# Kernel optimization log

Hardware: AMD Instinct MI355X
Metric: run time of the kernel (lower is better)

Reference implementation:

```python
import jax, jax.numpy as jnp
import numpy as np

B, S, D = 8, 1024, 1024
H, HD = 16, 64  # multiheads, head_dim; H*HD == D


def setup_inputs() -> dict:
    key = jax.random.key(0)
    ks = jax.random.split(key, 6)
    mk = lambda k, shape, scale=1.0: (jax.random.normal(k, shape, dtype=jnp.float32) * scale)
    return {
        "Q_seq": mk(ks[0], (B, S, D)),
        "K_seq": mk(ks[1], (B, S, D)),
        "V_seq": mk(ks[2], (B, S, D)),
        # nn.Linear weights stored as (out_features, in_features)
        "WQ": mk(ks[3], (H * HD, D), scale=D ** -0.5),
        "WK": mk(ks[4], (H * HD, D), scale=D ** -0.5),
        "WV": mk(ks[5], (H * HD, D), scale=D ** -0.5),
    }


def _attn(Q_seq, K_seq, V_seq, WQ, WK, WV):
    # projections (Linear: x @ W.T), then split heads -> [B, H, S, HD]
    def proj(x, W):
        y = jnp.einsum('bsd,od->bso', x, W)
        return y.reshape(x.shape[0], -1, H, HD).transpose(0, 2, 1, 3)
    Q, K, V = proj(Q_seq, WQ), proj(K_seq, WK), proj(V_seq, WV)
    scale = 1.0 / jnp.sqrt(jnp.float32(HD))
    scores = jnp.einsum('bhqd,bhkd->bhqk', Q, K) * scale  # [B,H,S,S]
    attn = jax.nn.softmax(scores, axis=-1)
    # dropout p=0.1 is identity in eval mode
    out = jnp.einsum('bhqk,bhkd->bhqd', attn, V)
    return out.transpose(0, 2, 1, 3).reshape(out.shape[0], -1, H * HD)


def reference(Q_seq, K_seq, V_seq, WQ, WK, WV):
    return _attn(Q_seq, K_seq, V_seq, WQ, WK, WV)
```

## Files before the change

### kernel.cpp

```cpp
#include <hip/hip_runtime.h>
#include <stdint.h>


#define B_N 8
#define S_N 1024
#define D_N 1024
#define H_N 16
#define HD_N 64
#define M_N (B_N * S_N)

typedef __bf16 bfrag __attribute__((ext_vector_type(8)));
typedef float f32x2 __attribute__((ext_vector_type(2)));
typedef float f32x4 __attribute__((ext_vector_type(4)));
typedef float f32x16 __attribute__((ext_vector_type(16)));
typedef unsigned int u32;
typedef u32 u32x2 __attribute__((ext_vector_type(2)));
typedef u32 u32x4 __attribute__((ext_vector_type(4)));
typedef unsigned short u16;

__device__ __forceinline__ u16 f2bf(float f) {
  uint32_t u = __float_as_uint(f);
  u += 0x7FFFu + ((u >> 16) & 1u);
  return (u16)(u >> 16);
}

__device__ __forceinline__ void gl_lds16(const void* g, void* l) {
  __builtin_amdgcn_global_load_lds(
      (const __attribute__((address_space(1))) uint32_t*)g,
      (__attribute__((address_space(3))) uint32_t*)l, 16, 0, 0);
}

__device__ __forceinline__ u32 cvtpk(float lo, float hi) {
  u32 r;
  asm("v_cvt_pk_bf16_f32 %0, %1, %2" : "=v"(r) : "v"(lo), "v"(hi));
  return r;
}

__device__ __forceinline__ float exp2r(float x) {
#if __has_builtin(__builtin_amdgcn_exp2f)
  return __builtin_amdgcn_exp2f(x);
#else
  float r;
  asm("v_exp_f32 %0, %1" : "=v"(r) : "v"(x));
  return r;
#endif
}

__device__ __forceinline__ f32x2 mk2(float x, float y) {
  f32x2 r; r[0] = x; r[1] = y; return r;
}
__device__ __forceinline__ f32x2 emax2(f32x2 a, f32x2 b) {
#if __has_builtin(__builtin_elementwise_max)
  return __builtin_elementwise_max(a, b);
#else
  return mk2(fmaxf(a[0], b[0]), fmaxf(a[1], b[1]));
#endif
}

__device__ __forceinline__ u32x2 pl32swap(u32 a, u32 b) {
#if __has_builtin(__builtin_amdgcn_permlane32_swap)
  return __builtin_amdgcn_permlane32_swap(a, b, false, false);
#else
  u32 sa = (u32)__shfl_xor((int)a, 32, 64), sb = (u32)__shfl_xor((int)b, 32, 64);
  const bool hi = (threadIdx.x & 32) != 0;
  u32x2 r;
  r[0] = hi ? sb : a;
  r[1] = hi ? b : sa;
  return r;
#endif
}

__device__ __forceinline__ float xhalf_max(float v) {
  u32x2 r = pl32swap(__float_as_uint(v), __float_as_uint(v));
  return fmaxf(__uint_as_float(r[0]), __uint_as_float(r[1]));
}
__device__ __forceinline__ float xhalf_add(float v) {
  u32x2 r = pl32swap(__float_as_uint(v), __float_as_uint(v));
  return __uint_as_float(r[0]) + __uint_as_float(r[1]);
}

__global__ __launch_bounds__(512, 1) void gemm_qkv(
    const float* __restrict__ Qs, const float* __restrict__ Ks,
    const float* __restrict__ Vs, const float* __restrict__ WQ,
    const float* __restrict__ WK, const float* __restrict__ WV,
    u16* __restrict__ Ybf) {
  const int bid = blockIdx.x;
  const int wid = (bid & 7) * 96 + (bid >> 3);
  const int mat = wid >> 8;
  const int rem = wid & 255;
  const int m0 = (rem >> 3) * 256;
  const int n0 = (rem & 7) * 128;

  const float* A = mat == 0 ? Qs : (mat == 1 ? Ks : Vs);
  const float* Bw = mat == 0 ? WQ : (mat == 1 ? WK : WV);
  u16* Y = Ybf + (size_t)mat * (M_N * D_N);

  __shared__ u16 Ast[2][4][4096];
  __shared__ u16 Bst[2][2][4096];

  const int t = threadIdx.x;
  const int w = t >> 6, l = t & 63;
  const int lr = l & 15, lg = l >> 4;
  const int wm = w >> 1, wn = w & 1;

  const float* aSrc = A + (size_t)(m0 + (t >> 3)) * D_N + (t & 7) * 8;
  const float* bSrc = Bw + (size_t)(n0 + (t >> 3)) * D_N + (t & 7) * 8;
  const int dst8 = (t >> 3) * 64 + ((((t & 7) ^ ((t >> 3) & 7))) << 3);

  const int asw = (lr & 7) << 3;
  const int koff0 = (lg * 8) ^ asw;
  const int koff1 = (32 + lg * 8) ^ asw;

  float4 ra[4][2], rw[2][2];

#define LOADT(tt)                                                             \
  do {                                                                        \
    _Pragma("unroll") for (int c_ = 0; c_ < 4; ++c_) {                        \
      ra[c_][0] = *(const float4*)(aSrc + (size_t)(c_ * 64) * D_N + (tt)*64); \
      ra[c_][1] =                                                             \
          *(const float4*)(aSrc + (size_t)(c_ * 64) * D_N + (tt)*64 + 4);     \
    }                                                                         \
    _Pragma("unroll") for (int c_ = 0; c_ < 2; ++c_) {                        \
      rw[c_][0] = *(const float4*)(bSrc + (size_t)(c_ * 64) * D_N + (tt)*64); \
      rw[c_][1] =                                                             \
          *(const float4*)(bSrc + (size_t)(c_ * 64) * D_N + (tt)*64 + 4);     \
    }                                                                         \
  } while (0)
#define WRITET(buf)                                                           \
  do {                                                                        \
    _Pragma("unroll") for (int c_ = 0; c_ < 4; ++c_) {                        \
      u32x4 pk_;                                                              \
      pk_[0] = cvtpk(ra[c_][0].x, ra[c_][0].y);                               \
      pk_[1] = cvtpk(ra[c_][0].z, ra[c_][0].w);                               \
      pk_[2] = cvtpk(ra[c_][1].x, ra[c_][1].y);                               \
      pk_[3] = cvtpk(ra[c_][1].z, ra[c_][1].w);                               \
      *(u32x4*)(&Ast[buf][c_][dst8]) = pk_;                                   \
    }                                                                         \
    _Pragma("unroll") for (int c_ = 0; c_ < 2; ++c_) {                        \
      u32x4 pk_;                                                              \
      pk_[0] = cvtpk(rw[c_][0].x, rw[c_][0].y);                               \
      pk_[1] = cvtpk(rw[c_][0].z, rw[c_][0].w);                               \
      pk_[2] = cvtpk(rw[c_][1].x, rw[c_][1].y);                               \
      pk_[3] = cvtpk(rw[c_][1].z, rw[c_][1].w);                               \
      *(u32x4*)(&Bst[buf][c_][dst8]) = pk_;                                   \
    }                                                                         \
  } while (0)
#define LDA8(AR, buf)                                                         \
  do {                                                                        \
    const u16* p_ = &Ast[buf][wm][lr * 64];                                   \
    _Pragma("unroll") for (int mf_ = 0; mf_ < 4; ++mf_) {                     \
      AR[mf_][0] = *(const bfrag*)(p_ + mf_ * 1024 + koff0);                  \
      AR[mf_][1] = *(const bfrag*)(p_ + mf_ * 1024 + koff1);                  \
    }                                                                         \
  } while (0)
#define LDB4(BR, buf, h)                                                      \
  do {                                                                        \
    const u16* p_ = &Bst[buf][wn][((h)*32 + lr) * 64];                        \
    BR[0][0] = *(const bfrag*)(p_ + koff0);                                   \
    BR[0][1] = *(const bfrag*)(p_ + koff1);                                   \
    BR[1][0] = *(const bfrag*)(p_ + 1024 + koff0);                            \
    BR[1][1] = *(const bfrag*)(p_ + 1024 + koff1);                            \
  } while (0)
#define MMAH(h, AR, BR)                                                       \
  do {                                                                        \
    __builtin_amdgcn_s_setprio(1);                                            \
    _Pragma("unroll") for (int mf_ = 0; mf_ < 4; ++mf_)                       \
    _Pragma("unroll") for (int j_ = 0; j_ < 2; ++j_)                          \
    _Pragma("unroll") for (int kk_ = 0; kk_ < 2; ++kk_)                       \
      acc[mf_][(h)*2 + j_] = __builtin_amdgcn_mfma_f32_16x16x32_bf16(         \
          AR[mf_][kk_], BR[j_][kk_], acc[mf_][(h)*2 + j_], 0, 0, 0);          \
    __builtin_amdgcn_s_setprio(0);                                            \
  } while (0)
#define BARR()                                                                \
  __builtin_amdgcn_s_barrier();                                               \
  __builtin_amdgcn_sched_barrier(0)
#define WAITL()                                                               \
  asm volatile("s_waitcnt lgkmcnt(0)" ::: "memory");                          \
  __builtin_amdgcn_sched_barrier(0)
#define WAITV0()                                                              \
  asm volatile("s_waitcnt vmcnt(0)" ::: "memory");                            \
  __builtin_amdgcn_sched_barrier(0)

  f32x4 acc[4][4];
#pragma unroll
  for (int i = 0; i < 4; ++i)
#pragma unroll
    for (int j = 0; j < 4; ++j) acc[i][j] = (f32x4){0.f, 0.f, 0.f, 0.f};

  LOADT(0);
  WAITV0();
  WRITET(0);
  LOADT(1);
  WAITL();
  BARR();

  for (int kt = 0; kt < 16; ++kt) {
    const int cb = kt & 1;
    bfrag a[4][2], b[2][2];
    LDA8(a, cb);
    LDB4(b, cb, 0);
    WAITL();
    MMAH(0, a, b);
    if (kt < 15) {
      WAITV0();
      WRITET(cb ^ 1);
      if (kt < 14) LOADT(kt + 2);
    }
    LDB4(b, cb, 1);
    WAITL();
    MMAH(1, a, b);
    BARR();
  }

  const float alpha = (mat == 0) ? 0.18033688011112042f : 1.0f;
  const int mrow = m0 + wm * 64;
  const int ncol = n0 + wn * 64;
  if (mat < 2) {
#pragma unroll
    for (int mf = 0; mf < 4; ++mf) {
      const int row0 = mrow + mf * 16 + lg * 4;
#pragma unroll
      for (int nf = 0; nf < 4; ++nf) {
        const int col = ncol + nf * 16 + lr;
#pragma unroll
        for (int r = 0; r < 4; ++r)
          Y[(size_t)(row0 + r) * D_N + col] = f2bf(acc[mf][nf][r] * alpha);
      }
    }
  } else {
    const int b = m0 >> 10;
#pragma unroll
    for (int mf = 0; mf < 4; ++mf) {
      const int s0 = (m0 & 1023) + wm * 64 + mf * 16 + lg * 4;
#pragma unroll
      for (int nf = 0; nf < 4; ++nf) {
        const int col = ncol + nf * 16 + lr;
        const f32x4 v = acc[mf][nf];
        ushort4 pk;
        pk.x = f2bf(v[0]); pk.y = f2bf(v[1]);
        pk.z = f2bf(v[2]); pk.w = f2bf(v[3]);
        *(ushort4*)(Y + (size_t)(b * D_N + col) * S_N + s0) = pk;
      }
    }
  }
#undef LOADT
#undef WRITET
#undef LDA8
#undef LDB4
#undef MMAH
#undef BARR
#undef WAITL
#undef WAITV0
}

union AttnSMem {
  struct { u16 K[3][4096]; u16 V[3][4096]; } st;
  float ol[4][32 * 34];
};

__global__ __launch_bounds__(256, 3) void attn_fwd(const u16* __restrict__ Yq,
                                                   const u16* __restrict__ Yk,
                                                   const u16* __restrict__ Yv,
                                                   float* __restrict__ out) {
  const int bid = blockIdx.x;
  const int wid = (bid & 7) * 128 + (bid >> 3);
  const int qt = wid & 7, bh = wid >> 3;
  const int b = bh >> 4, h = bh & 15;
  const int t = threadIdx.x, w = t >> 6, l = t & 63;
  const int ln = l & 31, hi = l >> 5;

  __shared__ AttnSMem sm;

  const int qbase = qt * 128 + w * 32;

  const int row0 = w * 8 + (l >> 3);
  const int srcoff = (((l & 7) ^ ((l >> 3) & 7)) << 3);
  const u16* kS0 = Yk + ((size_t)(b * S_N + row0) * D_N + h * HD_N + srcoff);
  const u16* vS0 = Yv + ((size_t)(b * D_N + h * HD_N + row0) * S_N + srcoff);

#define STAGE(buf, tt)                                                        \
  do {                                                                        \
    const u16* ka_ = kS0 + (size_t)(tt) * 64 * D_N;                           \
    const u16* va_ = vS0 + (tt) * 64;                                         \
    gl_lds16(ka_, sm.st.K[buf] + w * 512);                                    \
    gl_lds16(ka_ + (size_t)32 * D_N, sm.st.K[buf] + 2048 + w * 512);          \
    gl_lds16(va_, sm.st.V[buf] + w * 512);                                    \
    gl_lds16(va_ + (size_t)32 * S_N, sm.st.V[buf] + 2048 + w * 512);          \
  } while (0)

  bfrag qf[4];
  {
    const u16* qp = Yq + ((size_t)(b * S_N + qbase + ln) * D_N + h * HD_N + hi * 8);
#pragma unroll
    for (int c = 0; c < 4; ++c) qf[c] = *(const bfrag*)(qp + c * 16);
  }

  STAGE(0, 0);
  STAGE(1, 1);

  int kcol[4];
#pragma unroll
  for (int c = 0; c < 4; ++c)
    kcol[c] = (((c * 32 + hi * 16) ^ ((ln & 7) << 4)) >> 1);

  f32x16 o0, o1;
#pragma unroll
  for (int r = 0; r < 16; ++r) { o0[r] = 0.f; o1[r] = 0.f; }
  float m_r = -3.0e38f, l_r = 0.f;

  asm volatile("s_waitcnt vmcnt(4)" ::: "memory");
  __builtin_amdgcn_sched_barrier(0);
  __builtin_amdgcn_s_barrier();

  int rd = 0, sb = 2;
  for (int kt = 0; kt < 16; ++kt) {
    if (kt < 14) STAGE(sb, kt + 2);

    const u16* Kb = sm.st.K[rd];
    const u16* Vb = sm.st.V[rd];

    bfrag kf[8];
#pragma unroll
    for (int s2 = 0; s2 < 2; ++s2)
#pragma unroll
      for (int c = 0; c < 4; ++c)
        kf[s2 * 4 + c] = *(const bfrag*)(Kb + (s2 * 32 + ln) * 64 + kcol[c]);

    f32x16 sa, sbv;
#pragma unroll
    for (int r = 0; r < 16; ++r) { sa[r] = 0.f; sbv[r] = 0.f; }
    __builtin_amdgcn_s_setprio(1);
#pragma unroll
    for (int c = 0; c < 4; ++c) {
      sa = __builtin_amdgcn_mfma_f32_32x32x16_bf16(kf[c], qf[c], sa, 0, 0, 0);
      sbv = __builtin_amdgcn_mfma_f32_32x32x16_bf16(kf[4 + c], qf[c], sbv, 0, 0, 0);
    }
    __builtin_amdgcn_s_setprio(0);

    bfrag vf[8];
#pragma unroll
    for (int hf = 0; hf < 2; ++hf)
#pragma unroll
      for (int c = 0; c < 4; ++c)
        vf[hf * 4 + c] = *(const bfrag*)(Vb + (hf * 32 + ln) * 64 + kcol[c]);

    f32x2 t8[8];
#pragma unroll
    for (int r = 0; r < 8; ++r)
      t8[r] = emax2(mk2(sa[2 * r], sa[2 * r + 1]),
                    mk2(sbv[2 * r], sbv[2 * r + 1]));
#pragma unroll
    for (int r = 0; r < 4; ++r) t8[r] = emax2(t8[r], t8[r + 4]);
    t8[0] = emax2(t8[0], t8[2]);
    t8[1] = emax2(t8[1], t8[3]);
    t8[0] = emax2(t8[0], t8[1]);
    float pmax = fmaxf(t8[0][0], t8[0][1]);
    pmax = xhalf_max(pmax);

    if (__any(pmax > m_r + 8.f)) {
      const float mnew = fmaxf(m_r, pmax);
      const float corr = exp2r(m_r - mnew);
      const f32x2 cc = mk2(corr, corr);
#pragma unroll
      for (int r = 0; r < 8; ++r) {
        f32x2 v0 = mk2(o0[2 * r], o0[2 * r + 1]) * cc;
        f32x2 v1 = mk2(o1[2 * r], o1[2 * r + 1]) * cc;
        o0[2 * r] = v0[0]; o0[2 * r + 1] = v0[1];
        o1[2 * r] = v1[0]; o1[2 * r + 1] = v1[1];
      }
      l_r *= corr;
      m_r = mnew;
    }

#pragma unroll
    for (int r = 0; r < 16; ++r) sa[r] = exp2r(sa[r] - m_r);
#pragma unroll
    for (int r = 0; r < 16; ++r) sbv[r] = exp2r(sbv[r] - m_r);
    f32x2 s8v[8];
#pragma unroll
    for (int r = 0; r < 8; ++r)
      s8v[r] = mk2(sa[2 * r], sa[2 * r + 1]) + mk2(sbv[2 * r], sbv[2 * r + 1]);
#pragma unroll
    for (int r = 0; r < 4; ++r) s8v[r] = s8v[r] + s8v[r + 4];
    s8v[0] = s8v[0] + s8v[2];
    s8v[1] = s8v[1] + s8v[3];
    s8v[0] = s8v[0] + s8v[1];
    float rsum = s8v[0][0] + s8v[0][1];
    l_r += xhalf_add(rsum);

    __builtin_amdgcn_s_setprio(1);
#pragma unroll
    for (int c = 0; c < 4; ++c) {
      const int bs = (c & 1) * 8;
      float p0, p1, p2, p3, p4, p5, p6, p7;
      if (c < 2) {
        p0 = sa[bs + 0]; p1 = sa[bs + 1]; p2 = sa[bs + 2]; p3 = sa[bs + 3];
        p4 = sa[bs + 4]; p5 = sa[bs + 5]; p6 = sa[bs + 6]; p7 = sa[bs + 7];
      } else {
        p0 = sbv[bs + 0]; p1 = sbv[bs + 1]; p2 = sbv[bs + 2]; p3 = sbv[bs + 3];
        p4 = sbv[bs + 4]; p5 = sbv[bs + 5]; p6 = sbv[bs + 6]; p7 = sbv[bs + 7];
      }
      const u32 x1 = cvtpk(p0, p1), x2 = cvtpk(p2, p3);
      const u32 y1 = cvtpk(p4, p5), y2 = cvtpk(p6, p7);
      const u32x2 s1 = pl32swap(x1, y1);
      const u32x2 s2 = pl32swap(x2, y2);
      union { u32 u[4]; bfrag v; } pu;
      pu.u[0] = s1[0]; pu.u[1] = s2[0]; pu.u[2] = s1[1]; pu.u[3] = s2[1];
      o0 = __builtin_amdgcn_mfma_f32_32x32x16_bf16(vf[c], pu.v, o0, 0, 0, 0);
      o1 = __builtin_amdgcn_mfma_f32_32x32x16_bf16(vf[4 + c], pu.v, o1, 0, 0, 0);
    }
    __builtin_amdgcn_s_setprio(0);

    if (kt < 14) {
      asm volatile("s_waitcnt vmcnt(4)" ::: "memory");
    } else {
      asm volatile("s_waitcnt vmcnt(0)" ::: "memory");
    }
    __builtin_amdgcn_sched_barrier(0);
    __builtin_amdgcn_s_barrier();

    rd = (rd == 2) ? 0 : rd + 1;
    sb = (sb == 2) ? 0 : sb + 1;
  }

  const float inv = 1.f / l_r;
  float* ow = sm.ol[w];
  const int qr = l >> 1, ch = l & 1;
  const float* rp = ow + qr * 34 + ch * 16;
  float* op = out + ((size_t)(b * S_N + qbase + qr) * D_N + h * HD_N + ch * 16);

#pragma unroll
  for (int g = 0; g < 4; ++g) {
    f32x4 v;
#pragma unroll
    for (int j = 0; j < 4; ++j) v[j] = o0[g * 4 + j] * inv;
    *(f32x4*)(ow + ln * 34 + g * 8 + hi * 4) = v;
  }
  asm volatile("s_waitcnt lgkmcnt(0)" ::: "memory");
  __builtin_amdgcn_sched_barrier(0);
#pragma unroll
  for (int j = 0; j < 4; ++j)
    *(f32x4*)(op + j * 4) = *(const f32x4*)(rp + j * 4);
  asm volatile("s_waitcnt lgkmcnt(0)" ::: "memory");
  __builtin_amdgcn_sched_barrier(0);

#pragma unroll
  for (int g = 0; g < 4; ++g) {
    f32x4 v;
#pragma unroll
    for (int j = 0; j < 4; ++j) v[j] = o1[g * 4 + j] * inv;
    *(f32x4*)(ow + ln * 34 + g * 8 + hi * 4) = v;
  }
  asm volatile("s_waitcnt lgkmcnt(0)" ::: "memory");
  __builtin_amdgcn_sched_barrier(0);
#pragma unroll
  for (int j = 0; j < 4; ++j)
    *(f32x4*)(op + 32 + j * 4) = *(const f32x4*)(rp + j * 4);
#undef STAGE
}

extern "C" void kernel_launch(void* const* d_in, const int* in_sizes, int n_in,
                              void* d_out, int out_size, void* d_ws, size_t ws_size,
                              hipStream_t stream) {
  const float* Qs = (const float*)d_in[0];
  const float* Ks = (const float*)d_in[1];
  const float* Vs = (const float*)d_in[2];
  const float* WQ = (const float*)d_in[3];
  const float* WK = (const float*)d_in[4];
  const float* WV = (const float*)d_in[5];
  if (ws_size < 50331648ull) return;

  u16* Ybf = (u16*)d_ws;
  float* out = (float*)d_out;

  gemm_qkv<<<dim3(768), 512, 0, stream>>>(Qs, Ks, Vs, WQ, WK, WV, Ybf);
  attn_fwd<<<dim3(1024), 256, 0, stream>>>(Ybf, Ybf + 8388608, Ybf + 16777216, out);
}
```

Before: 145.4 us.

## Process two query sub-tiles per wave in attention to reuse K/V fragments

Each attention wave now handles 64 query rows (two 32-row sub-tiles with separate online-softmax state) instead of 32. This halves the grid and halves the K/V staging and LDS fragment reads per query row. The cost is roughly doubled register use, so launch bounds drop from 3 to 2 blocks per CU, and there are fewer blocks (512) to fill the GPU. Separately, the GEMM loop now issues the next tile's global-to-LDS writes and loads before the first MMA half rather than after it.

```diff
diff --git a/kernel.cpp b/kernel.cpp
--- a/kernel.cpp
+++ b/kernel.cpp
@@ -199,13 +199,13 @@
     bfrag a[4][2], b[2][2];
     LDA8(a, cb);
     LDB4(b, cb, 0);
-    WAITL();
-    MMAH(0, a, b);
     if (kt < 15) {
       WAITV0();
       WRITET(cb ^ 1);
       if (kt < 14) LOADT(kt + 2);
     }
+    WAITL();
+    MMAH(0, a, b);
     LDB4(b, cb, 1);
     WAITL();
     MMAH(1, a, b);
@@ -258,20 +258,90 @@
   float ol[4][32 * 34];
 };
 
-__global__ __launch_bounds__(256, 3) void attn_fwd(const u16* __restrict__ Yq,
+__device__ __forceinline__ void sm_pv(f32x16& sa, f32x16& sbv, float& m_r,
+                                      float& l_r, f32x16& oA, f32x16& oB,
+                                      const bfrag* vf) {
+  f32x2 t8[8];
+#pragma unroll
+  for (int r = 0; r < 8; ++r)
+    t8[r] = emax2(mk2(sa[2 * r], sa[2 * r + 1]),
+                  mk2(sbv[2 * r], sbv[2 * r + 1]));
+#pragma unroll
+  for (int r = 0; r < 4; ++r) t8[r] = emax2(t8[r], t8[r + 4]);
+  t8[0] = emax2(t8[0], t8[2]);
+  t8[1] = emax2(t8[1], t8[3]);
+  t8[0] = emax2(t8[0], t8[1]);
+  float pmax = fmaxf(t8[0][0], t8[0][1]);
+  pmax = xhalf_max(pmax);
+
+  if (__any(pmax > m_r + 8.f)) {
+    const float mnew = fmaxf(m_r, pmax);
+    const float corr = exp2r(m_r - mnew);
+    const f32x2 cc = mk2(corr, corr);
+#pragma unroll
+    for (int r = 0; r < 8; ++r) {
+      f32x2 v0 = mk2(oA[2 * r], oA[2 * r + 1]) * cc;
+      f32x2 v1 = mk2(oB[2 * r], oB[2 * r + 1]) * cc;
+      oA[2 * r] = v0[0]; oA[2 * r + 1] = v0[1];
+      oB[2 * r] = v1[0]; oB[2 * r + 1] = v1[1];
+    }
+    l_r *= corr;
+    m_r = mnew;
+  }
+
+#pragma unroll
+  for (int r = 0; r < 16; ++r) sa[r] = exp2r(sa[r] - m_r);
+#pragma unroll
+  for (int r = 0; r < 16; ++r) sbv[r] = exp2r(sbv[r] - m_r);
+  f32x2 s8v[8];
+#pragma unroll
+  for (int r = 0; r < 8; ++r)
+    s8v[r] = mk2(sa[2 * r], sa[2 * r + 1]) + mk2(sbv[2 * r], sbv[2 * r + 1]);
+#pragma unroll
+  for (int r = 0; r < 4; ++r) s8v[r] = s8v[r] + s8v[r + 4];
+  s8v[0] = s8v[0] + s8v[2];
+  s8v[1] = s8v[1] + s8v[3];
+  s8v[0] = s8v[0] + s8v[1];
+  l_r += xhalf_add(s8v[0][0] + s8v[0][1]);
+
+  __builtin_amdgcn_s_setprio(1);
+#pragma unroll
+  for (int c = 0; c < 4; ++c) {
+    const int bs = (c & 1) * 8;
+    float p0, p1, p2, p3, p4, p5, p6, p7;
+    if (c < 2) {
+      p0 = sa[bs + 0]; p1 = sa[bs + 1]; p2 = sa[bs + 2]; p3 = sa[bs + 3];
+      p4 = sa[bs + 4]; p5 = sa[bs + 5]; p6 = sa[bs + 6]; p7 = sa[bs + 7];
+    } else {
+      p0 = sbv[bs + 0]; p1 = sbv[bs + 1]; p2 = sbv[bs + 2]; p3 = sbv[bs + 3];
+      p4 = sbv[bs + 4]; p5 = sbv[bs + 5]; p6 = sbv[bs + 6]; p7 = sbv[bs + 7];
+    }
+    const u32 x1 = cvtpk(p0, p1), x2 = cvtpk(p2, p3);
+    const u32 y1 = cvtpk(p4, p5), y2 = cvtpk(p6, p7);
+    const u32x2 s1 = pl32swap(x1, y1);
+    const u32x2 s2 = pl32swap(x2, y2);
+    union { u32 u[4]; bfrag v; } pu;
+    pu.u[0] = s1[0]; pu.u[1] = s2[0]; pu.u[2] = s1[1]; pu.u[3] = s2[1];
+    oA = __builtin_amdgcn_mfma_f32_32x32x16_bf16(vf[c], pu.v, oA, 0, 0, 0);
+    oB = __builtin_amdgcn_mfma_f32_32x32x16_bf16(vf[4 + c], pu.v, oB, 0, 0, 0);
+  }
+  __builtin_amdgcn_s_setprio(0);
+}
+
+__global__ __launch_bounds__(256, 2) void attn_fwd(const u16* __restrict__ Yq,
                                                    const u16* __restrict__ Yk,
                                                    const u16* __restrict__ Yv,
                                                    float* __restrict__ out) {
   const int bid = blockIdx.x;
-  const int wid = (bid & 7) * 128 + (bid >> 3);
-  const int qt = wid & 7, bh = wid >> 3;
+  const int wid = (bid & 7) * 64 + (bid >> 3);
+  const int qt = wid & 3, bh = wid >> 2;
   const int b = bh >> 4, h = bh & 15;
   const int t = threadIdx.x, w = t >> 6, l = t & 63;
   const int ln = l & 31, hi = l >> 5;
 
   __shared__ AttnSMem sm;
 
-  const int qbase = qt * 128 + w * 32;
+  const int qbase = qt * 256 + w * 64;
 
   const int row0 = w * 8 + (l >> 3);
   const int srcoff = (((l & 7) ^ ((l >> 3) & 7)) << 3);
@@ -288,11 +358,14 @@
     gl_lds16(va_ + (size_t)32 * S_N, sm.st.V[buf] + 2048 + w * 512);          \
   } while (0)
 
-  bfrag qf[4];
+  bfrag qf0[4], qf1[4];
   {
     const u16* qp = Yq + ((size_t)(b * S_N + qbase + ln) * D_N + h * HD_N + hi * 8);
 #pragma unroll
-    for (int c = 0; c < 4; ++c) qf[c] = *(const bfrag*)(qp + c * 16);
+    for (int c = 0; c < 4; ++c) qf0[c] = *(const bfrag*)(qp + c * 16);
+    const u16* qp1 = qp + (size_t)32 * D_N;
+#pragma unroll
+    for (int c = 0; c < 4; ++c) qf1[c] = *(const bfrag*)(qp1 + c * 16);
   }
 
   STAGE(0, 0);
@@ -303,10 +376,10 @@
   for (int c = 0; c < 4; ++c)
     kcol[c] = (((c * 32 + hi * 16) ^ ((ln & 7) << 4)) >> 1);
 
-  f32x16 o0, o1;
-#pragma unroll
-  for (int r = 0; r < 16; ++r) { o0[r] = 0.f; o1[r] = 0.f; }
-  float m_r = -3.0e38f, l_r = 0.f;
+  f32x16 o00, o01, o10, o11;
+#pragma unroll
+  for (int r = 0; r < 16; ++r) { o00[r] = 0.f; o01[r] = 0.f; o10[r] = 0.f; o11[r] = 0.f; }
+  float m0r = -3.0e38f, l0r = 0.f, m1r = -3.0e38f, l1r = 0.f;
 
   asm volatile("s_waitcnt vmcnt(4)" ::: "memory");
   __builtin_amdgcn_sched_barrier(0);
@@ -326,14 +399,16 @@
       for (int c = 0; c < 4; ++c)
         kf[s2 * 4 + c] = *(const bfrag*)(Kb + (s2 * 32 + ln) * 64 + kcol[c]);
 
-    f32x16 sa, sbv;
-#pragma unroll
-    for (int r = 0; r < 16; ++r) { sa[r] = 0.f; sbv[r] = 0.f; }
+    f32x16 sa0, sb0, sa1, sb1;
+#pragma unroll
+    for (int r = 0; r < 16; ++r) { sa0[r] = 0.f; sb0[r] = 0.f; sa1[r] = 0.f; sb1[r] = 0.f; }
     __builtin_amdgcn_s_setprio(1);
 #pragma unroll
     for (int c = 0; c < 4; ++c) {
-      sa = __builtin_amdgcn_mfma_f32_32x32x16_bf16(kf[c], qf[c], sa, 0, 0, 0);
-      sbv = __builtin_amdgcn_mfma_f32_32x32x16_bf16(kf[4 + c], qf[c], sbv, 0, 0, 0);
+      sa0 = __builtin_amdgcn_mfma_f32_32x32x16_bf16(kf[c], qf0[c], sa0, 0, 0, 0);
+      sb0 = __builtin_amdgcn_mfma_f32_32x32x16_bf16(kf[4 + c], qf0[c], sb0, 0, 0, 0);
+      sa1 = __builtin_amdgcn_mfma_f32_32x32x16_bf16(kf[c], qf1[c], sa1, 0, 0, 0);
+      sb1 = __builtin_amdgcn_mfma_f32_32x32x16_bf16(kf[4 + c], qf1[c], sb1, 0, 0, 0);
     }
     __builtin_amdgcn_s_setprio(0);
 
@@ -344,72 +419,8 @@
       for (int c = 0; c < 4; ++c)
         vf[hf * 4 + c] = *(const bfrag*)(Vb + (hf * 32 + ln) * 64 + kcol[c]);
 
-    f32x2 t8[8];
-#pragma unroll
-    for (int r = 0; r < 8; ++r)
-      t8[r] = emax2(mk2(sa[2 * r], sa[2 * r + 1]),
-                    mk2(sbv[2 * r], sbv[2 * r + 1]));
-#pragma unroll
-    for (int r = 0; r < 4; ++r) t8[r] = emax2(t8[r], t8[r + 4]);
-    t8[0] = emax2(t8[0], t8[2]);
-    t8[1] = emax2(t8[1], t8[3]);
-    t8[0] = emax2(t8[0], t8[1]);
-    float pmax = fmaxf(t8[0][0], t8[0][1]);
-    pmax = xhalf_max(pmax);
-
-    if (__any(pmax > m_r + 8.f)) {
-      const float mnew = fmaxf(m_r, pmax);
-      const float corr = exp2r(m_r - mnew);
-      const f32x2 cc = mk2(corr, corr);
-#pragma unroll
-      for (int r = 0; r < 8; ++r) {
-        f32x2 v0 = mk2(o0[2 * r], o0[2 * r + 1]) * cc;
-        f32x2 v1 = mk2(o1[2 * r], o1[2 * r + 1]) * cc;
-        o0[2 * r] = v0[0]; o0[2 * r + 1] = v0[1];
-        o1[2 * r] = v1[0]; o1[2 * r + 1] = v1[1];
-      }
-      l_r *= corr;
-      m_r = mnew;
-    }
-
-#pragma unroll
-    for (int r = 0; r < 16; ++r) sa[r] = exp2r(sa[r] - m_r);
-#pragma unroll
-    for (int r = 0; r < 16; ++r) sbv[r] = exp2r(sbv[r] - m_r);
-    f32x2 s8v[8];
-#pragma unroll
-    for (int r = 0; r < 8; ++r)
-      s8v[r] = mk2(sa[2 * r], sa[2 * r + 1]) + mk2(sbv[2 * r], sbv[2 * r + 1]);
-#pragma unroll
-    for (int r = 0; r < 4; ++r) s8v[r] = s8v[r] + s8v[r + 4];
-    s8v[0] = s8v[0] + s8v[2];
-    s8v[1] = s8v[1] + s8v[3];
-    s8v[0] = s8v[0] + s8v[1];
-    float rsum = s8v[0][0] + s8v[0][1];
-    l_r += xhalf_add(rsum);
-
-    __builtin_amdgcn_s_setprio(1);
-#pragma unroll
-    for (int c = 0; c < 4; ++c) {
-      const int bs = (c & 1) * 8;
-      float p0, p1, p2, p3, p4, p5, p6, p7;
-      if (c < 2) {
-        p0 = sa[bs + 0]; p1 = sa[bs + 1]; p2 = sa[bs + 2]; p3 = sa[bs + 3];
-        p4 = sa[bs + 4]; p5 = sa[bs + 5]; p6 = sa[bs + 6]; p7 = sa[bs + 7];
-      } else {
-        p0 = sbv[bs + 0]; p1 = sbv[bs + 1]; p2 = sbv[bs + 2]; p3 = sbv[bs + 3];
-        p4 = sbv[bs + 4]; p5 = sbv[bs + 5]; p6 = sbv[bs + 6]; p7 = sbv[bs + 7];
-      }
-      const u32 x1 = cvtpk(p0, p1), x2 = cvtpk(p2, p3);
-      const u32 y1 = cvtpk(p4, p5), y2 = cvtpk(p6, p7);
-      const u32x2 s1 = pl32swap(x1, y1);
-      const u32x2 s2 = pl32swap(x2, y2);
-      union { u32 u[4]; bfrag v; } pu;
-      pu.u[0] = s1[0]; pu.u[1] = s2[0]; pu.u[2] = s1[1]; pu.u[3] = s2[1];
-      o0 = __builtin_amdgcn_mfma_f32_32x32x16_bf16(vf[c], pu.v, o0, 0, 0, 0);
-      o1 = __builtin_amdgcn_mfma_f32_32x32x16_bf16(vf[4 + c], pu.v, o1, 0, 0, 0);
-    }
-    __builtin_amdgcn_s_setprio(0);
+    sm_pv(sa0, sb0, m0r, l0r, o00, o01, vf);
+    sm_pv(sa1, sb1, m1r, l1r, o10, o11, vf);
 
     if (kt < 14) {
       asm volatile("s_waitcnt vmcnt(4)" ::: "memory");
@@ -423,39 +434,37 @@
     sb = (sb == 2) ? 0 : sb + 1;
   }
 
-  const float inv = 1.f / l_r;
   float* ow = sm.ol[w];
   const int qr = l >> 1, ch = l & 1;
   const float* rp = ow + qr * 34 + ch * 16;
-  float* op = out + ((size_t)(b * S_N + qbase + qr) * D_N + h * HD_N + ch * 16);
-
-#pragma unroll
-  for (int g = 0; g < 4; ++g) {
-    f32x4 v;
-#pragma unroll
-    for (int j = 0; j < 4; ++j) v[j] = o0[g * 4 + j] * inv;
-    *(f32x4*)(ow + ln * 34 + g * 8 + hi * 4) = v;
-  }
-  asm volatile("s_waitcnt lgkmcnt(0)" ::: "memory");
-  __builtin_amdgcn_sched_barrier(0);
-#pragma unroll
-  for (int j = 0; j < 4; ++j)
-    *(f32x4*)(op + j * 4) = *(const f32x4*)(rp + j * 4);
-  asm volatile("s_waitcnt lgkmcnt(0)" ::: "memory");
-  __builtin_amdgcn_sched_barrier(0);
-
-#pragma unroll
-  for (int g = 0; g < 4; ++g) {
-    f32x4 v;
-#pragma unroll
-    for (int j = 0; j < 4; ++j) v[j] = o1[g * 4 + j] * inv;
-    *(f32x4*)(ow + ln * 34 + g * 8 + hi * 4) = v;
-  }
-  asm volatile("s_waitcnt lgkmcnt(0)" ::: "memory");
-  __builtin_amdgcn_sched_barrier(0);
-#pragma unroll
-  for (int j = 0; j < 4; ++j)
-    *(f32x4*)(op + 32 + j * 4) = *(const f32x4*)(rp + j * 4);
+
+#define EPI(OH, INV, GROW, COL0)                                              \
+  do {                                                                        \
+    _Pragma("unroll") for (int g_ = 0; g_ < 4; ++g_) {                        \
+      f32x4 v_;                                                               \
+      _Pragma("unroll") for (int j_ = 0; j_ < 4; ++j_)                        \
+          v_[j_] = OH[g_ * 4 + j_] * (INV);                                   \
+      *(f32x4*)(ow + ln * 34 + g_ * 8 + hi * 4) = v_;                         \
+    }                                                                         \
+    asm volatile("s_waitcnt lgkmcnt(0)" ::: "memory");                        \
+    __builtin_amdgcn_sched_barrier(0);                                        \
+    {                                                                         \
+      float* op_ = out + ((size_t)(b * S_N + qbase + (GROW) + qr) * D_N +     \
+                          h * HD_N + ch * 16 + (COL0));                       \
+      _Pragma("unroll") for (int j_ = 0; j_ < 4; ++j_)                        \
+          *(f32x4*)(op_ + j_ * 4) = *(const f32x4*)(rp + j_ * 4);             \
+    }                                                                         \
+    asm volatile("s_waitcnt lgkmcnt(0)" ::: "memory");                        \
+    __builtin_amdgcn_sched_barrier(0);                                        \
+  } while (0)
+
+  const float inv0 = 1.f / l0r;
+  const float inv1 = 1.f / l1r;
+  EPI(o00, inv0, 0, 0);
+  EPI(o01, inv0, 0, 32);
+  EPI(o10, inv1, 32, 0);
+  EPI(o11, inv1, 32, 32);
+#undef EPI
 #undef STAGE
 }
 
@@ -474,5 +483,5 @@
   float* out = (float*)d_out;
 
   gemm_qkv<<<dim3(768), 512, 0, stream>>>(Qs, Ks, Vs, WQ, WK, WV, Ybf);
-  attn_fwd<<<dim3(1024), 256, 0, stream>>>(Ybf, Ybf + 8388608, Ybf + 16777216, out);
-}
+  attn_fwd<<<dim3(512), 256, 0, stream>>>(Ybf, Ybf + 8388608, Ybf + 16777216, out);
+}
```

New measurement: 144.8 us. About the same (-0.4%).
